# Performance work log

Hardware: AMD Instinct MI355X
Metric: run time of the kernel (lower is better)

## Reference

```python
import jax, jax.numpy as jnp
import numpy as np

LOCAL_REGION = 16
GRANULARITY = 2048
INIT_RATIO = 8
EXPAND_RATIO = 2
C = 128
N_LAYERS = 5


def setup_inputs() -> dict:
    key = jax.random.key(0)
    ks = jax.random.split(key, 20)
    g = lambda k, s: jax.random.normal(k, s, dtype=jnp.float32) * 0.05
    z = lambda n: jnp.zeros((n,), jnp.float32)
    return {
        "batch_x": jax.random.normal(ks[0], (1, 16384, 4), dtype=jnp.float32),
        # PT: attr embedding (in_channel=1 -> 128), positional MLP (3->128->128)
        "attr_w": g(ks[1], (1, C)), "attr_b": z(C),
        "pos_w1": g(ks[2], (3, C)), "pos_b1": z(C),
        "pos_w2": g(ks[3], (C, C)), "pos_b2": z(C),
        # 5 self-attention layers over the K-neighborhood
        "wq": g(ks[4], (N_LAYERS, C, C)),
        "wk": g(ks[5], (N_LAYERS, C, C)),
        "wv": g(ks[6], (N_LAYERS, C, C)),
        "wout": g(ks[7], (C, C)), "bout": z(C),
        # mu/sigma head: 128 -> 64 -> 16 -> 2
        "ms_w1": g(ks[8], (C, 64)), "ms_b1": z(64),
        "ms_w2": g(ks[9], (64, 16)), "ms_b2": z(16),
        "ms_w3": g(ks[10], (16, 2)), "ms_b3": z(2),
    }


def _window_schedule(N):
    base = min(N // INIT_RATIO, GRANULARITY)
    win = base
    sched = []
    cursor = base
    while cursor < N:
        win = min(win * EXPAND_RATIO, GRANULARITY)
        sched.append((cursor, min(win, N - cursor)))
        cursor += win
    return sched


def _forward(batch_x, attr_w, attr_b, pos_w1, pos_b1, pos_w2, pos_b2,
             wq, wk, wv, wout, bout, ms_w1, ms_b1, ms_w2, ms_b2, ms_w3, ms_b3):
    B, N, _ = batch_x.shape
    total_bits = jnp.float32(0.0)
    for cur, w in _window_schedule(N):
        context = batch_x[:, :cur, :]
        target = batch_x[:, cur:cur + w, :]
        tg, ta = target[..., :3], target[..., 3:]    # [B,M,3], [B,M,1]
        cg, ca = context[..., :3], context[..., 3:]  # [B,Nc,3], [B,Nc,1]
        # knn_points: brute-force squared distances, K smallest
        d2 = (jnp.sum(tg * tg, -1)[:, :, None] + jnp.sum(cg * cg, -1)[:, None, :]
              - 2.0 * jnp.einsum('bmd,bnd->bmn', tg, cg))  # [B,M,Nc]
        _, idx = jax.lax.top_k(-d2, LOCAL_REGION)            # [B,M,K]
        # knn_gather
        gg = jnp.take_along_axis(cg[:, None], idx[..., None], axis=2)  # [B,M,K,3]
        ga = jnp.take_along_axis(ca[:, None], idx[..., None], axis=2)  # [B,M,K,1]
        # n_scale_ball: center each neighborhood, scale into unit ball
        gg = gg - jnp.mean(gg, axis=2, keepdims=True)
        r = jnp.max(jnp.linalg.norm(gg, axis=-1, keepdims=True), axis=2, keepdims=True)
        gg = gg / jnp.maximum(r, 1e-8)
        # PT: pos-encoded grouped self-attention, max-pool over K
        pos = jax.nn.relu(gg @ pos_w1 + pos_b1) @ pos_w2 + pos_b2  # [B,M,K,C]
        f = ga @ attr_w + attr_b + pos
        for l in range(N_LAYERS):
            q, k, v = f @ wq[l], f @ wk[l], f @ wv[l]
            a = jax.nn.softmax(jnp.einsum('bmkc,bmjc->bmkj', q, k)
                               / jnp.sqrt(jnp.float32(C)), axis=-1)
            f = f + jnp.einsum('bmkj,bmjc->bmkc', a, v)
        feat = jnp.max(f @ wout + bout, axis=2)  # [B,M,C]
        # mu/sigma head
        h = jax.nn.relu(feat @ ms_w1 + ms_b1)
        h = jax.nn.relu(h @ ms_w2 + ms_b2)
        ms = h @ ms_w3 + ms_b3
        mu, sigma = ms[..., :1], jnp.exp(ms[..., 1:])
        # feature_probs_based_mu_sigma: bits under quantized Gaussian
        inv = 1.0 / (sigma * jnp.sqrt(jnp.float32(2.0)))
        probs = 0.5 * (jax.lax.erf((ta + 0.5 - mu) * inv)
                       - jax.lax.erf((ta - 0.5 - mu) * inv))
        total_bits = total_bits + jnp.sum(jnp.clip(-jnp.log2(probs + 1e-10), 0.0, 50.0))
    return total_bits


def reference(batch_x, attr_w, attr_b, pos_w1, pos_b1, pos_w2, pos_b2,
              wq, wk, wv, wout, bout, ms_w1, ms_b1, ms_w2, ms_b2, ms_w3, ms_b3):
    return _forward(batch_x, attr_w, attr_b, pos_w1, pos_b1, pos_w2, pos_b2,
                    wq, wk, wv, wout, bout, ms_w1, ms_b1, ms_w2, ms_b2, ms_w3, ms_b3)
```

## Files before the change

kernel.cpp:

```cpp
#include <hip/hip_runtime.h>
#include <math.h>

#define NPTS 16384
#define WWIN 2048
#define NWIN 7
#define KNB  16
#define CDIM 128
#define NTGT (NPTS - WWIN)
#define TPB  4
#define NBLK (NTGT / TPB)
#define NMAT 12

typedef _Float16 f16;
typedef __attribute__((ext_vector_type(8))) _Float16 f16x8;
typedef __attribute__((ext_vector_type(4))) _Float16 f16x4;
typedef __attribute__((ext_vector_type(2))) _Float16 f16x2;
typedef __attribute__((ext_vector_type(4))) float f32x4;

#define MFMA16(a, b, c)  __builtin_amdgcn_mfma_f32_16x16x32_f16((a), (b), (c), 0, 0, 0)
#define MFMA16H(a, b, c) __builtin_amdgcn_mfma_f32_16x16x16f16((a), (b), (c), 0, 0, 0)

__device__ __forceinline__ unsigned umax_(unsigned a, unsigned b) { return a > b ? a : b; }
__device__ __forceinline__ unsigned umin_(unsigned a, unsigned b) { return a < b ? a : b; }

__global__ void prep_kernel(const float* __restrict__ pos_w2,
                            const float* __restrict__ wq,
                            const float* __restrict__ wk,
                            const float* __restrict__ wv,
                            const float* __restrict__ wout,
                            f16* __restrict__ wt) {
  const int i = blockIdx.x * 256 + threadIdx.x;
  if (i >= NMAT * 16384) return;
  const int mat = i >> 14;
  const int e   = i & 16383;
  const int k   = e >> 7;
  const int n   = e & 127;
  if (mat < 7) {
    const float* src = (mat == 0) ? pos_w2 : (mat <= 5 ? wv + (mat - 1) * 16384 : wout);
    wt[mat * 16384 + n * 128 + k] = (f16)src[k * 128 + n];
  } else {
    const int l = mat - 7;
    const float* qr = wq + l * 16384 + k * 128;
    const float* kr = wk + l * 16384 + n * 128;
    float sacc = 0.f;
#pragma unroll 4
    for (int c = 0; c < 128; ++c) sacc += qr[c] * kr[c];
    wt[mat * 16384 + n * 128 + k] = (f16)sacc;
  }
}

__device__ __forceinline__ f16x8 ldA(const f16* __restrict__ buf, int row0,
                                     int l15, int lg, int kc) {
  const int row = row0 + l15;
  const int col = (kc * 32 + lg * 8) ^ ((row & 7) << 3);
  return *(const f16x8*)(buf + row * 128 + col);
}

__device__ __forceinline__ void stD(f16* __restrict__ buf, int row0, int col0,
                                    int l15, int lg, const f32x4 v) {
#pragma unroll
  for (int r = 0; r < 4; ++r) {
    const int row = row0 + lg * 4 + r;
    const int col = (col0 + l15) ^ ((row & 7) << 3);
    buf[row * 128 + col] = (f16)v[r];
  }
}

__device__ __forceinline__ void gemm_half(const f16* __restrict__ src,
                                          const f16* __restrict__ wmat,
                                          int l15, int lg, int ncol,
                                          f32x4 (&acc)[4]) {
#pragma unroll
  for (int kc = 0; kc < 4; ++kc) {
    const f16x8 b = *(const f16x8*)(wmat + (ncol + l15) * 128 + kc * 32 + lg * 8);
#pragma unroll
    for (int mt = 0; mt < 4; ++mt) {
      const f16x8 a = ldA(src, mt * 16, l15, lg, kc);
      acc[mt] = MFMA16(a, b, acc[mt]);
    }
  }
}

__global__ __launch_bounds__(256, 3)
void nn_kernel(
    const float4* __restrict__ bx, const f16* __restrict__ wt,
    const float* __restrict__ attr_w, const float* __restrict__ attr_b,
    const float* __restrict__ pos_w1, const float* __restrict__ pos_b1,
    const float* __restrict__ pos_b2, const float* __restrict__ bout,
    const float* __restrict__ ms_w1, const float* __restrict__ ms_b1,
    const float* __restrict__ ms_w2, const float* __restrict__ ms_b2,
    const float* __restrict__ ms_w3, const float* __restrict__ ms_b3,
    float* __restrict__ partials) {
  __shared__ __align__(16) f16 fA[64 * 128];
  __shared__ __align__(16) f16 qA[64 * 128];
  __shared__ __align__(16) char aux[4096];

  const int t     = threadIdx.x;
  const int wv    = t >> 6;
  const int lane  = t & 63;
  const int l15   = lane & 15;
  const int lg    = lane >> 4;
  const int n0    = wv * 32;
  const int slot0 = (NBLK - 1 - blockIdx.x) * TPB;

  f16* pAh = (f16*)aux;
  unsigned* nbr = (unsigned*)aux;
  float* ggs = (float*)(aux + 1024);

  {
    const int  slot = slot0 + wv;
    const int  cur  = WWIN * ((slot0 >> 11) + 1);
    const float4 tp = bx[WWIN + slot];

    unsigned u0 = 0xFFFFFFF0u, u1 = 0xFFFFFFF1u, u2 = 0xFFFFFFF2u, u3 = 0xFFFFFFF3u;

#define INS4(P) { const unsigned p_ = (P);                                     \
    const unsigned t0 = umax_(u0, p_); u0 = umin_(u0, p_);                     \
    const unsigned t1 = umax_(u1, t0); u1 = umin_(u1, t0);                     \
    const unsigned t2 = umax_(u2, t1); u2 = umin_(u2, t1);                     \
    u3 = umin_(u3, t2); }
#define PROC(CA, CB, JJ) {                                                     \
    const float dx0 = tp.x - (CA).x, dy0 = tp.y - (CA).y, dz0 = tp.z - (CA).z; \
    const float dx1 = tp.x - (CB).x, dy1 = tp.y - (CB).y, dz1 = tp.z - (CB).z; \
    const float d20 = dx0 * dx0 + dy0 * dy0 + dz0 * dz0;                       \
    const float d21 = dx1 * dx1 + dy1 * dy1 + dz1 * dz1;                       \
    const unsigned p0 = ((__float_as_uint(d20) << 1) & 0xFFFFC000u) | (unsigned)(JJ);      \
    const unsigned p1 = ((__float_as_uint(d21) << 1) & 0xFFFFC000u) | (unsigned)((JJ) + 64); \
    INS4(p0) INS4(p1) }

    float4 a0 = bx[lane],       b0 = bx[lane + 64];
    float4 a1 = bx[lane + 128], b1 = bx[lane + 192];
    float4 a2 = bx[lane + 256], b2 = bx[lane + 320];
    float4 a3 = bx[lane + 384], b3 = bx[lane + 448];
    for (int j = lane; j < cur; j += 512) {
      const float4 n0_ = bx[j + 512], n1_ = bx[j + 576];
      const float4 n2_ = bx[j + 640], n3_ = bx[j + 704];
      const float4 n4_ = bx[j + 768], n5_ = bx[j + 832];
      const float4 n6_ = bx[j + 896], n7_ = bx[j + 960];
      PROC(a0, b0, j)       a0 = n0_; b0 = n1_;
      PROC(a1, b1, j + 128) a1 = n2_; b1 = n3_;
      PROC(a2, b2, j + 256) a2 = n4_; b2 = n5_;
      PROC(a3, b3, j + 384) a3 = n6_; b3 = n7_;
    }
#undef PROC
#undef INS4

    for (int n = 0; n < 16; ++n) {
      unsigned m = u0;
      m = umin_(m, (unsigned)__shfl_xor((int)m, 1));
      m = umin_(m, (unsigned)__shfl_xor((int)m, 2));
      m = umin_(m, (unsigned)__shfl_xor((int)m, 4));
      m = umin_(m, (unsigned)__shfl_xor((int)m, 8));
      m = umin_(m, (unsigned)__shfl_xor((int)m, 16));
      m = umin_(m, (unsigned)__shfl_xor((int)m, 32));
      if (lane == n) nbr[wv * 16 + n] = m & 0x3FFFu;
      if (u0 == m) { u0 = u1; u1 = u2; u2 = u3; u3 = 0xFFFFFFFFu; }
    }
  }
  __syncthreads();

  if (t < 64) {
    const int nid  = (int)nbr[t];
    const float4 p = bx[nid];
    float sx = p.x, sy = p.y, sz = p.z;
#pragma unroll
    for (int m = 1; m < 16; m <<= 1) {
      sx += __shfl_xor(sx, m); sy += __shfl_xor(sy, m); sz += __shfl_xor(sz, m);
    }
    const float gx = p.x - sx * 0.0625f;
    const float gy = p.y - sy * 0.0625f;
    const float gz = p.z - sz * 0.0625f;
    float nr = sqrtf(gx * gx + gy * gy + gz * gz);
#pragma unroll
    for (int m = 1; m < 16; m <<= 1) nr = fmaxf(nr, __shfl_xor(nr, m));
    const float inv = 1.f / fmaxf(nr, 1e-8f);
    ggs[t * 4 + 0] = gx * inv; ggs[t * 4 + 1] = gy * inv;
    ggs[t * 4 + 2] = gz * inv; ggs[t * 4 + 3] = p.w;
  }
  __syncthreads();

  {
    const int row = t & 63;
    const int cb  = (t >> 6) * 32;
    const float gx = ggs[row * 4], gy = ggs[row * 4 + 1], gz = ggs[row * 4 + 2];
#pragma unroll
    for (int c = cb; c < cb + 32; c += 2) {
      const float h0 = pos_b1[c]     + gx * pos_w1[c]     + gy * pos_w1[128 + c]     + gz * pos_w1[256 + c];
      const float h1 = pos_b1[c + 1] + gx * pos_w1[c + 1] + gy * pos_w1[128 + c + 1] + gz * pos_w1[256 + c + 1];
      f16x2 pr; pr[0] = (f16)fmaxf(h0, 0.f); pr[1] = (f16)fmaxf(h1, 0.f);
      *(f16x2*)(qA + row * 128 + (c ^ ((row & 7) << 3))) = pr;
    }
  }
  __syncthreads();

  {
#pragma unroll
    for (int nt = 0; nt < 2; ++nt) {
      f32x4 acc[4];
#pragma unroll
      for (int mt = 0; mt < 4; ++mt) acc[mt] = (f32x4){0.f, 0.f, 0.f, 0.f};
      gemm_half(qA, wt, l15, lg, n0 + nt * 16, acc);
      const int col = n0 + nt * 16 + l15;
      const float bias = pos_b2[col] + attr_b[col];
      const float aw   = attr_w[col];
#pragma unroll
      for (int mt = 0; mt < 4; ++mt) {
#pragma unroll
        for (int r = 0; r < 4; ++r)
          acc[mt][r] += bias + ggs[(mt * 16 + lg * 4 + r) * 4 + 3] * aw;
        stD(fA, mt * 16, n0 + nt * 16, l15, lg, acc[mt]);
      }
    }
  }
  __syncthreads();

  for (int l = 0; l < 5; ++l) {
    f16x4 vfrag[2][4];
    {
#pragma unroll
      for (int nt = 0; nt < 2; ++nt) {
        f32x4 acc[4];
#pragma unroll
        for (int mt = 0; mt < 4; ++mt) acc[mt] = (f32x4){0.f, 0.f, 0.f, 0.f};
        gemm_half(fA, wt + (7 + l) * 16384, l15, lg, n0 + nt * 16, acc);
#pragma unroll
        for (int mt = 0; mt < 4; ++mt)
          stD(qA, mt * 16, n0 + nt * 16, l15, lg, acc[mt]);
      }
#pragma unroll
      for (int nt = 0; nt < 2; ++nt) {
        f32x4 acc[4];
#pragma unroll
        for (int mt = 0; mt < 4; ++mt) acc[mt] = (f32x4){0.f, 0.f, 0.f, 0.f};
        gemm_half(fA, wt + (1 + l) * 16384, l15, lg, n0 + nt * 16, acc);
#pragma unroll
        for (int mt = 0; mt < 4; ++mt)
#pragma unroll
          for (int r = 0; r < 4; ++r) vfrag[nt][mt][r] = (f16)acc[mt][r];
      }
    }
    __syncthreads();
    {
      f32x4 s = (f32x4){0.f, 0.f, 0.f, 0.f};
#pragma unroll
      for (int kc = 0; kc < 4; ++kc)
        s = MFMA16(ldA(qA, wv * 16, l15, lg, kc), ldA(fA, wv * 16, l15, lg, kc), s);
#pragma unroll
      for (int r = 0; r < 4; ++r) {
        float v = s[r] * 0.08838834764831844055f;
        float mx = v;
#pragma unroll
        for (int m = 1; m < 16; m <<= 1) mx = fmaxf(mx, __shfl_xor(mx, m));
        const float e = __expf(v - mx);
        float sm = e;
#pragma unroll
        for (int m = 1; m < 16; m <<= 1) sm += __shfl_xor(sm, m);
        pAh[wv * 256 + (lg * 4 + r) * 16 + l15] = (f16)(e / sm);
      }
    }
    __syncthreads();
    {
#pragma unroll
      for (int tt = 0; tt < 4; ++tt) {
        const f16x4 aP = *(const f16x4*)(pAh + tt * 256 + l15 * 16 + lg * 4);
#pragma unroll
        for (int nt = 0; nt < 2; ++nt) {
          f32x4 c;
#pragma unroll
          for (int r = 0; r < 4; ++r) {
            const int row = tt * 16 + lg * 4 + r;
            const int col = (n0 + nt * 16 + l15) ^ ((row & 7) << 3);
            c[r] = (float)fA[row * 128 + col];
          }
          c = MFMA16H(aP, vfrag[nt][tt], c);
          stD(fA, tt * 16, n0 + nt * 16, l15, lg, c);
        }
      }
    }
    __syncthreads();
  }

  float* feats = (float*)aux;
  float* h1s   = feats + 512;
  float* h2s   = h1s + 256;
  float* btmp  = h2s + 64;
  {
#pragma unroll
    for (int nt = 0; nt < 2; ++nt) {
      f32x4 acc[4];
#pragma unroll
      for (int mt = 0; mt < 4; ++mt) acc[mt] = (f32x4){0.f, 0.f, 0.f, 0.f};
      gemm_half(fA, wt + 6 * 16384, l15, lg, n0 + nt * 16, acc);
      const int col = n0 + nt * 16 + l15;
      const float bo = bout[col];
#pragma unroll
      for (int mt = 0; mt < 4; ++mt) {
        const f32x4 v = acc[mt];
        float m = fmaxf(fmaxf(v[0], v[1]), fmaxf(v[2], v[3])) + bo;
        m = fmaxf(m, __shfl_xor(m, 16));
        m = fmaxf(m, __shfl_xor(m, 32));
        if (lg == 0) feats[mt * 128 + col] = m;
      }
    }
  }
  __syncthreads();
  {
    const int tt = t >> 6, h = t & 63;
    float a = ms_b1[h];
#pragma unroll 4
    for (int c = 0; c < 128; ++c) a += feats[tt * 128 + c] * ms_w1[c * 64 + h];
    h1s[tt * 64 + h] = fmaxf(a, 0.f);
  }
  __syncthreads();
  if (t < 64) {
    const int tt = t >> 4, h = t & 15;
    float a = ms_b2[h];
#pragma unroll 4
    for (int c = 0; c < 64; ++c) a += h1s[tt * 64 + c] * ms_w2[c * 16 + h];
    h2s[tt * 16 + h] = fmaxf(a, 0.f);
  }
  __syncthreads();
  if (t < TPB) {
    float mu = ms_b3[0], lgs = ms_b3[1];
#pragma unroll
    for (int c = 0; c < 16; ++c) {
      mu  += h2s[t * 16 + c] * ms_w3[2 * c];
      lgs += h2s[t * 16 + c] * ms_w3[2 * c + 1];
    }
    const float sigma = expf(lgs);
    const float inv   = 1.f / (sigma * 1.41421356237309504880f);
    const float ta    = ((const float*)bx)[(WWIN + slot0 + t) * 4 + 3];
    const float p = 0.5f * (erff((ta + 0.5f - mu) * inv) - erff((ta - 0.5f - mu) * inv));
    float bits = -log2f(p + 1e-10f);
    btmp[t] = fminf(fmaxf(bits, 0.f), 50.f);
  }
  __syncthreads();
  if (t == 0) partials[blockIdx.x] = btmp[0] + btmp[1] + btmp[2] + btmp[3];
}

__global__ void reduce_kernel(const float* __restrict__ partials, float* __restrict__ out) {
  float s = 0.f;
  for (int i = threadIdx.x; i < NBLK; i += 256) s += partials[i];
#pragma unroll
  for (int m = 1; m < 64; m <<= 1) s += __shfl_xor(s, m);
  __shared__ float wsum[4];
  if ((threadIdx.x & 63) == 0) wsum[threadIdx.x >> 6] = s;
  __syncthreads();
  if (threadIdx.x == 0) out[0] = wsum[0] + wsum[1] + wsum[2] + wsum[3];
}

extern "C" void kernel_launch(void* const* d_in, const int* in_sizes, int n_in,
                              void* d_out, int out_size, void* d_ws, size_t ws_size,
                              hipStream_t stream) {
  const float4* bx     = (const float4*)d_in[0];
  const float* attr_w  = (const float*)d_in[1];
  const float* attr_b  = (const float*)d_in[2];
  const float* pos_w1  = (const float*)d_in[3];
  const float* pos_b1  = (const float*)d_in[4];
  const float* pos_w2  = (const float*)d_in[5];
  const float* pos_b2  = (const float*)d_in[6];
  const float* wq      = (const float*)d_in[7];
  const float* wk      = (const float*)d_in[8];
  const float* wv      = (const float*)d_in[9];
  const float* wout    = (const float*)d_in[10];
  const float* bout    = (const float*)d_in[11];
  const float* ms_w1   = (const float*)d_in[12];
  const float* ms_b1   = (const float*)d_in[13];
  const float* ms_w2   = (const float*)d_in[14];
  const float* ms_b2   = (const float*)d_in[15];
  const float* ms_w3   = (const float*)d_in[16];
  const float* ms_b3   = (const float*)d_in[17];

  f16*   wt       = (f16*)((char*)d_ws);
  float* partials = (float*)((char*)d_ws + (1u << 19));

  prep_kernel<<<(NMAT * 16384 + 255) / 256, 256, 0, stream>>>(pos_w2, wq, wk, wv, wout, wt);
  nn_kernel<<<NBLK, 256, 0, stream>>>(bx, wt, attr_w, attr_b,
                                      pos_w1, pos_b1, pos_b2, bout,
                                      ms_w1, ms_b1, ms_w2, ms_b2, ms_w3, ms_b3,
                                      partials);
  reduce_kernel<<<1, 256, 0, stream>>>(partials, (float*)d_out);
}
```

Before: 362.3 us.

## Fuse V projection into per-wave attention output, drop one barrier

The V projection, previously computed cooperatively across waves as column slices and kept in registers, is now computed by each wave for its own 16-row neighborhood over all 128 columns, then immediately consumed by the attention-times-V MFMA. This removes one block-wide __syncthreads per layer and lets each wave apply attention to its own rows without cross-wave dependence. The A fragments of features are loaded once and reused for both QK^T and V. It changes the work split: weight fragments are read straight from global memory in the inner loop, and per-wave register pressure shifts.

```diff
diff --git a/kernel.cpp b/kernel.cpp
--- a/kernel.cpp
+++ b/kernel.cpp
@@ -215,7 +215,6 @@
   __syncthreads();
 
   for (int l = 0; l < 5; ++l) {
-    f16x4 vfrag[2][4];
     {
 #pragma unroll
       for (int nt = 0; nt < 2; ++nt) {
@@ -227,24 +226,16 @@
         for (int mt = 0; mt < 4; ++mt)
           stD(qA, mt * 16, n0 + nt * 16, l15, lg, acc[mt]);
       }
-#pragma unroll
-      for (int nt = 0; nt < 2; ++nt) {
-        f32x4 acc[4];
-#pragma unroll
-        for (int mt = 0; mt < 4; ++mt) acc[mt] = (f32x4){0.f, 0.f, 0.f, 0.f};
-        gemm_half(fA, wt + (1 + l) * 16384, l15, lg, n0 + nt * 16, acc);
-#pragma unroll
-        for (int mt = 0; mt < 4; ++mt)
-#pragma unroll
-          for (int r = 0; r < 4; ++r) vfrag[nt][mt][r] = (f16)acc[mt][r];
-      }
     }
     __syncthreads();
     {
+      f16x8 af[4];
+#pragma unroll
+      for (int kc = 0; kc < 4; ++kc) af[kc] = ldA(fA, wv * 16, l15, lg, kc);
       f32x4 s = (f32x4){0.f, 0.f, 0.f, 0.f};
 #pragma unroll
       for (int kc = 0; kc < 4; ++kc)
-        s = MFMA16(ldA(qA, wv * 16, l15, lg, kc), ldA(fA, wv * 16, l15, lg, kc), s);
+        s = MFMA16(ldA(qA, wv * 16, l15, lg, kc), af[kc], s);
 #pragma unroll
       for (int r = 0; r < 4; ++r) {
         float v = s[r] * 0.08838834764831844055f;
@@ -257,24 +248,28 @@
         for (int m = 1; m < 16; m <<= 1) sm += __shfl_xor(sm, m);
         pAh[wv * 256 + (lg * 4 + r) * 16 + l15] = (f16)(e / sm);
       }
-    }
-    __syncthreads();
-    {
-#pragma unroll
-      for (int tt = 0; tt < 4; ++tt) {
-        const f16x4 aP = *(const f16x4*)(pAh + tt * 256 + l15 * 16 + lg * 4);
-#pragma unroll
-        for (int nt = 0; nt < 2; ++nt) {
-          f32x4 c;
-#pragma unroll
-          for (int r = 0; r < 4; ++r) {
-            const int row = tt * 16 + lg * 4 + r;
-            const int col = (n0 + nt * 16 + l15) ^ ((row & 7) << 3);
-            c[r] = (float)fA[row * 128 + col];
-          }
-          c = MFMA16H(aP, vfrag[nt][tt], c);
-          stD(fA, tt * 16, n0 + nt * 16, l15, lg, c);
+      const f16x4 aP = *(const f16x4*)(pAh + wv * 256 + l15 * 16 + lg * 4);
+      const f16* wvm = wt + (1 + l) * 16384;
+#pragma unroll
+      for (int nt = 0; nt < 8; ++nt) {
+        f32x4 vacc = (f32x4){0.f, 0.f, 0.f, 0.f};
+#pragma unroll
+        for (int kc = 0; kc < 4; ++kc) {
+          const f16x8 b = *(const f16x8*)(wvm + (nt * 16 + l15) * 128 + kc * 32 + lg * 8);
+          vacc = MFMA16(af[kc], b, vacc);
         }
+        f16x4 vf;
+#pragma unroll
+        for (int r = 0; r < 4; ++r) vf[r] = (f16)vacc[r];
+        f32x4 c;
+#pragma unroll
+        for (int r = 0; r < 4; ++r) {
+          const int row = wv * 16 + lg * 4 + r;
+          const int col = (nt * 16 + l15) ^ ((row & 7) << 3);
+          c[r] = (float)fA[row * 128 + col];
+        }
+        c = MFMA16H(aP, vf, c);
+        stD(fA, wv * 16, nt * 16, l15, lg, c);
       }
     }
     __syncthreads();
```

Result: slower. 495.1 us (+36.6%).
